# Kernel optimization log

Hardware: AMD Instinct MI355X
Metric: run time of the kernel (lower is better)

## Reference

```python
import jax, jax.numpy as jnp
import numpy as np

THRESHOLD = 0.5     # overlap_thresh
NEG_POS = 3         # negative:positive ratio
VAR = (0.1, 0.2)    # cfg['variance']


def point_form(pr):
    # cxcywh -> xmin,ymin,xmax,ymax
    return jnp.concatenate([pr[:, :2] - pr[:, 2:] / 2, pr[:, :2] + pr[:, 2:] / 2], axis=1)


def jaccard(a, b):
    # a: [N,4] point-form truths, b: [P,4] point-form priors -> IoU [N,P]
    lt = jnp.maximum(a[:, None, :2], b[None, :, :2])
    rb = jnp.minimum(a[:, None, 2:], b[None, :, 2:])
    wh = jnp.clip(rb - lt, 0.0)
    inter = wh[..., 0] * wh[..., 1]
    area_a = ((a[:, 2] - a[:, 0]) * (a[:, 3] - a[:, 1]))[:, None]
    area_b = ((b[:, 2] - b[:, 0]) * (b[:, 3] - b[:, 1]))[None, :]
    return inter / (area_a + area_b - inter)


def encode(matched, priors):
    # matched: [P,4] point-form, priors: [P,4] cxcywh
    g_cxcy = ((matched[:, :2] + matched[:, 2:]) / 2 - priors[:, :2]) / (VAR[0] * priors[:, 2:])
    g_wh = jnp.log((matched[:, 2:] - matched[:, :2]) / priors[:, 2:]) / VAR[1]
    return jnp.concatenate([g_cxcy, g_wh], axis=1)


def match_one(truths, labels, priors):
    # truths [N,4], labels [N], priors [P,4] cxcywh
    N = truths.shape[0]
    P = priors.shape[0]
    overlaps = jaccard(truths, point_form(priors))          # [N,P]
    best_prior_idx = jnp.argmax(overlaps, axis=1)           # [N] best prior per truth
    best_truth_overlap = jnp.max(overlaps, axis=0)          # [P]
    best_truth_idx = jnp.argmax(overlaps, axis=0)           # [P]
    # ensure each truth's best prior is kept (overlap forced to 2)
    best_truth_overlap = best_truth_overlap.at[best_prior_idx].set(2.0)
    hit = best_prior_idx[:, None] == jnp.arange(P)[None, :]  # [N,P]
    chosen = jnp.max(jnp.where(hit, jnp.arange(N)[:, None], -1), axis=0)
    best_truth_idx = jnp.where(chosen >= 0, chosen, best_truth_idx)
    matched = truths[best_truth_idx]                        # [P,4]
    conf = labels[best_truth_idx].astype(jnp.int32) + 1
    conf = jnp.where(best_truth_overlap < THRESHOLD, 0, conf)
    return encode(matched, priors), conf


def smooth_l1(x):
    ax = jnp.abs(x)
    return jnp.where(ax < 1.0, 0.5 * ax * ax, ax - 0.5)


def multibox_loss(loc_data, conf_data, priors, targets):
    num, P, C = conf_data.shape
    truths = targets[..., :4]
    labels = targets[..., 4]
    loc_t, conf_t = jax.vmap(match_one, in_axes=(0, 0, None))(truths, labels, priors)
    pos = conf_t > 0                                        # [B,P]

    # localization loss over positives
    loss_l = jnp.sum(jnp.where(pos[..., None], smooth_l1(loc_data - loc_t), 0.0))

    # hard-negative mining score: logsumexp - conf[label clamped to {0,1}]
    batch_conf = jax.lax.stop_gradient(conf_data).reshape(-1, C)
    conf_flat = conf_t.reshape(-1)
    clamped = jnp.where(conf_flat != 0, 1, conf_flat)
    # replicate torch nonzero()-indexing quirk: row 0 also set to 1 if any positive exists
    clamped = clamped.at[0].set(jnp.where(jnp.any(conf_flat != 0), 1, clamped[0]))
    lse = jax.scipy.special.logsumexp(batch_conf, axis=1)
    loss_c = lse - jnp.take_along_axis(batch_conf, clamped[:, None], axis=1)[:, 0]
    loss_c = loss_c.reshape(num, P)
    loss_c = jnp.where(pos, 0.0, loss_c)
    # rank of each prior by descending mining loss
    idx_rank = jnp.argsort(jnp.argsort(-loss_c, axis=1), axis=1)
    num_pos = jnp.sum(pos.astype(jnp.int32), axis=1, keepdims=True)  # [B,1]
    num_neg = jnp.clip(NEG_POS * num_pos, None, P - 1)
    neg = idx_rank < num_neg
    sel = pos | neg

    # confidence cross-entropy over selected priors, original labels as targets
    logp = jax.nn.log_softmax(conf_data, axis=-1)           # [B,P,C]
    ce = -jnp.take_along_axis(logp, conf_t[..., None], axis=-1)[..., 0]
    loss_conf = jnp.sum(jnp.where(sel, ce, 0.0))

    Nf = jnp.sum(num_pos).astype(jnp.float32)
    return loss_l / Nf, loss_conf / Nf


def setup_inputs() -> dict:
    key = jax.random.key(0)
    k1, k2, k3, k4, k5, k6, k7 = jax.random.split(key, 7)
    B, P, C, NOBJ = 128, 8732, 21, 20
    loc_data = jax.random.normal(k1, (B, P, 4), jnp.float32)
    conf_data = jax.random.normal(k2, (B, P, C), jnp.float32)
    pcxy = jax.random.uniform(k3, (P, 2), jnp.float32, 0.05, 0.95)
    pwh = jax.random.uniform(k4, (P, 2), jnp.float32, 0.05, 0.4)
    priors = jnp.concatenate([pcxy, pwh], axis=1)           # cxcywh
    mins = jax.random.uniform(k5, (B, NOBJ, 2), jnp.float32, 0.0, 0.6)
    wh = jax.random.uniform(k6, (B, NOBJ, 2), jnp.float32, 0.05, 0.35)
    lab = jax.random.randint(k7, (B, NOBJ), 0, C - 1).astype(jnp.float32)
    targets = jnp.concatenate([mins, mins + wh, lab[..., None]], axis=-1)
    return {"loc_data": loc_data, "conf_data": conf_data, "priors": priors, "targets": targets}


def reference(loc_data, conf_data, priors, targets):
    return multibox_loss(loc_data, conf_data, priors, targets)
```

## Files before the change

kernel.cpp:

```cpp
#include <hip/hip_runtime.h>

#define PP 8732
#define NB 20
#define NC 21
#define BTH 256
#define NCH 35
#define BTS 1024
#define NWS (BTS/64)

__device__ __forceinline__ float sl1(float d){
  float a = fabsf(d);
  return a < 1.0f ? 0.5f*a*a : a - 0.5f;
}

__device__ __forceinline__ float wave_max64(float x){
  int t;
  t = __builtin_amdgcn_update_dpp(0, __float_as_int(x), 0x111, 0xF, 0xF, true); x = fmaxf(x, __int_as_float(t));
  t = __builtin_amdgcn_update_dpp(0, __float_as_int(x), 0x112, 0xF, 0xF, true); x = fmaxf(x, __int_as_float(t));
  t = __builtin_amdgcn_update_dpp(0, __float_as_int(x), 0x114, 0xF, 0xF, true); x = fmaxf(x, __int_as_float(t));
  t = __builtin_amdgcn_update_dpp(0, __float_as_int(x), 0x118, 0xF, 0xF, true); x = fmaxf(x, __int_as_float(t));
  t = __builtin_amdgcn_update_dpp(0, __float_as_int(x), 0x142, 0xF, 0xF, true); x = fmaxf(x, __int_as_float(t));
  t = __builtin_amdgcn_update_dpp(0, __float_as_int(x), 0x143, 0xF, 0xF, true); x = fmaxf(x, __int_as_float(t));
  return __int_as_float(__builtin_amdgcn_readlane(__float_as_int(x), 63));
}

extern "C" __global__ void __launch_bounds__(BTH)
mb_main(const float* __restrict__ conf_data,
        const float* __restrict__ priors,
        const float* __restrict__ targets,
        float* __restrict__ rankneg,
        unsigned char* __restrict__ meta,
        unsigned long long* __restrict__ keys2)
{
  const int b = blockIdx.x, chunk = blockIdx.y;
  const int tid = threadIdx.x, lane = tid & 63, wid = tid >> 6;
  const int q0 = chunk*BTH + wid*64;
  const int cnt = (q0 < PP) ? ((PP - q0 < 64) ? (PP - q0) : 64) : 0;

  __shared__ float s_buf[4][64*NC];
  __shared__ float4 s_tr4[NB];
  __shared__ unsigned long long s_keys[4][NB];

  if (tid < NB*4){
    int n = tid>>2, k2 = tid&3;
    ((float*)s_tr4)[tid] = targets[((long)b*NB + n)*5 + k2];
  }
  if (lane < NB) s_keys[wid][lane] = 0ULL;
  __syncthreads();

  if (cnt == 64){
    const float4* cb4 = reinterpret_cast<const float4*>(conf_data + ((long)b*PP + q0)*NC);
    float4* sb4 = reinterpret_cast<float4*>(s_buf[wid]);
    #pragma unroll
    for (int ii=0; ii<6; ii++){
      int i = ii*64 + lane;
      if (i < 336) sb4[i] = cb4[i];
    }
  } else if (cnt > 0){
    const float4* cb4 = reinterpret_cast<const float4*>(conf_data + ((long)b*PP + q0)*NC);
    float4* sb4 = reinterpret_cast<float4*>(s_buf[wid]);
    const int tot4 = (cnt*NC) >> 2;
    for (int i=lane; i<tot4; i+=64) sb4[i] = cb4[i];
  }

  const bool valid = (lane < cnt);
  const int p  = q0 + lane;
  const int pl = valid ? p : 0;

  const float* v = s_buf[wid] + lane*NC;
  float m = v[0];
  #pragma unroll
  for (int c=1;c<NC;c++) m = fmaxf(m, v[c]);
  float s = 0.f;
  #pragma unroll
  for (int c=0;c<NC;c++) s += __expf(v[c]-m);
  float lse = __logf(s) + m;
  if (valid) rankneg[(long)b*PP + p] = lse - v[0];

  float4 pr = reinterpret_cast<const float4*>(priors)[pl];
  float bx1 = pr.x - pr.z*0.5f, by1 = pr.y - pr.w*0.5f;
  float bx2 = pr.x + pr.z*0.5f, by2 = pr.y + pr.w*0.5f;
  float area_b = (bx2-bx1)*(by2-by1);
  float bestov = -1.0f; int bestn = 0;

  for (int n=0;n<NB;n++){
    float4 t = s_tr4[n];
    float lx=fmaxf(t.x,bx1), ly=fmaxf(t.y,by1);
    float rx=fminf(t.z,bx2), ry=fminf(t.w,by2);
    float iw=fmaxf(rx-lx,0.f), ih=fmaxf(ry-ly,0.f);
    float inter = iw*ih;
    float aa = (t.z-t.x)*(t.w-t.y);
    float iou = inter * __builtin_amdgcn_rcpf(aa + area_b - inter);
    if (iou > bestov){ bestov=iou; bestn=n; }

    float iouv = valid ? iou : -1.0f;
    float wmax = wave_max64(iouv);
    unsigned long long mk = __ballot(valid && (iou == wmax));
    if (mk){
      int wlane = __ffsll((long long)mk) - 1;
      if (lane == wlane)
        s_keys[wid][n] = ((unsigned long long)__float_as_uint(iou)<<32)
                       | (unsigned long long)(0xFFFFFFFFu - (unsigned)p);
    }
  }

  if (valid) meta[(long)b*PP + p] = (unsigned char)((bestn<<1) | (bestov >= 0.5f ? 1 : 0));

  __syncthreads();
  if (tid < NB){
    unsigned long long mx = s_keys[0][tid];
    #pragma unroll
    for (int w=1;w<4;w++) if (s_keys[w][tid] > mx) mx = s_keys[w][tid];
    keys2[((long)b*NCH + chunk)*NB + tid] = mx;
  }
}

extern "C" __global__ void __launch_bounds__(BTS)
mb_select(const float* __restrict__ loc_data,
          const float* __restrict__ conf_data,
          const float* __restrict__ priors,
          const float* __restrict__ targets,
          const float* __restrict__ rankneg,
          const unsigned char* __restrict__ meta,
          const unsigned long long* __restrict__ keys2,
          float* __restrict__ rowres, int* __restrict__ ticket,
          float* __restrict__ out, int Bn)
{
  const int b = blockIdx.x, tid = threadIdx.x, lane = tid & 63, wid = tid >> 6;
  __shared__ float s_val[PP];
  __shared__ unsigned int s_meta4[PP/4];
  __shared__ float4 s_tr4[NB];
  __shared__ float s_lab[NB];
  __shared__ int   s_bp[NB];
  __shared__ int   s_cnt[2][NWS];
  __shared__ float s_fa[NWS], s_fb[NWS], s_fc[NWS];
  __shared__ int   s_ia[NWS];
  __shared__ float s_rowll, s_rowpc, s_delta;
  __shared__ int   s_npos, s_spec, s_last;
  unsigned char* s_meta = (unsigned char*)s_meta4;
  float4* sv4 = reinterpret_cast<float4*>(s_val);

  const float4* rr = reinterpret_cast<const float4*>(rankneg + (long)b*PP);
  for (int i=tid;i<PP/4;i+=BTS) sv4[i]=rr[i];
  const unsigned int* mr = reinterpret_cast<const unsigned int*>(meta + (long)b*PP);
  for (int i=tid;i<PP/4;i+=BTS) s_meta4[i]=mr[i];
  if (tid < NB*5){
    int n = tid/5, k2 = tid-n*5;
    float vv = targets[((long)b*NB+n)*5+k2];
    if (k2<4) ((float*)&s_tr4[n])[k2]=vv; else s_lab[n]=vv;
  }
  if (tid < NB){
    unsigned long long mx = 0ULL;
    #pragma unroll
    for (int c=0;c<NCH;c++){
      unsigned long long kk = keys2[((long)b*NCH + c)*NB + tid];
      if (kk > mx) mx = kk;
    }
    s_bp[tid] = (int)(0xFFFFFFFFu - (unsigned)(mx & 0xFFFFFFFFULL));
  }
  if (tid==0){ s_spec=0; s_delta=0.f; }
  __syncthreads();

  if (tid==0){
    for (int n=0;n<NB;n++) s_meta[s_bp[n]] = (unsigned char)((n<<1)|1);
  }
  __syncthreads();

  float ll=0.f, pc=0.f; int np=0;
  for (int p=tid;p<PP;p+=BTS){
    int mt = s_meta[p];
    if (mt & 1){
      np++;
      int n = mt>>1;
      int ct = (int)s_lab[n] + 1;
      const float* cp = conf_data + ((long)b*PP+p)*NC;
      float v0 = cp[0], vct = cp[ct];
      pc += s_val[p] + v0 - vct;
      float4 t = s_tr4[n];
      float4 pr = reinterpret_cast<const float4*>(priors)[p];
      float4 ld = reinterpret_cast<const float4*>(loc_data)[(long)b*PP+p];
      float g0 = ((t.x+t.z)*0.5f - pr.x)/(0.1f*pr.z);
      float g1 = ((t.y+t.w)*0.5f - pr.y)/(0.1f*pr.w);
      float g2 = __logf((t.z-t.x)/pr.z)/0.2f;
      float g3 = __logf((t.w-t.y)/pr.w)/0.2f;
      ll += sl1(ld.x-g0)+sl1(ld.y-g1)+sl1(ld.z-g2)+sl1(ld.w-g3);
      s_val[p] = 0.f;
    } else if (b==0 && p==0){
      float v0 = conf_data[0], v1 = conf_data[1];
      float r0 = s_val[0];
      float r0p = r0 + v0 - v1;
      s_delta = r0 - r0p;
      s_spec = 1;
      s_val[0] = r0p;
    }
  }
  #pragma unroll
  for (int o=32;o;o>>=1){
    ll += __shfl_down(ll,o,64);
    pc += __shfl_down(pc,o,64);
    np += __shfl_down(np,o,64);
  }
  if (lane==0){ s_fa[wid]=ll; s_fb[wid]=pc; s_ia[wid]=np; }
  __syncthreads();

  float4 rv0 = sv4[tid];
  float4 rv1 = sv4[tid+1024];
  float4 rv2 = (tid < PP/4-2048) ? sv4[tid+2048]
                                 : make_float4(0.f,0.f,0.f,0.f);

  if (tid==0){
    float a=0.f,c2=0.f; int ni=0;
    for (int w=0;w<NWS;w++){ a+=s_fa[w]; c2+=s_fb[w]; ni+=s_ia[w]; }
    s_rowll=a; s_rowpc=c2; s_npos=ni;
  }
  __syncthreads();
  const int num_pos = s_npos;
  int k = num_pos*3; if (k > PP-1) k = PP-1;

  float negsum = 0.f;
  if (k > 0){
    unsigned lo=0u, hi=0x7f800000u;
    int it=0;
    while (lo < hi){
      unsigned mid = lo + ((hi - lo + 1u) >> 1);
      int c = (__float_as_uint(rv0.x)>=mid) + (__float_as_uint(rv0.y)>=mid)
            + (__float_as_uint(rv0.z)>=mid) + (__float_as_uint(rv0.w)>=mid)
            + (__float_as_uint(rv1.x)>=mid) + (__float_as_uint(rv1.y)>=mid)
            + (__float_as_uint(rv1.z)>=mid) + (__float_as_uint(rv1.w)>=mid)
            + (__float_as_uint(rv2.x)>=mid) + (__float_as_uint(rv2.y)>=mid)
            + (__float_as_uint(rv2.z)>=mid) + (__float_as_uint(rv2.w)>=mid);
      #pragma unroll
      for (int o=32;o;o>>=1) c += __shfl_down(c,o,64);
      int sl2 = it&1;
      if (lane==0) s_cnt[sl2][wid]=c;
      __syncthreads();
      int tot=0;
      #pragma unroll
      for (int w=0;w<NWS;w++) tot += s_cnt[sl2][w];
      if (tot >= k) lo = mid; else hi = mid - 1u;
      it++;
    }
    const unsigned vstar = lo;

    int cg=0; float sg=0.f;
    #define ACC(x) if (__float_as_uint(x)>vstar){cg++;sg+=(x);}
    ACC(rv0.x) ACC(rv0.y) ACC(rv0.z) ACC(rv0.w)
    ACC(rv1.x) ACC(rv1.y) ACC(rv1.z) ACC(rv1.w)
    ACC(rv2.x) ACC(rv2.y) ACC(rv2.z) ACC(rv2.w)
    #undef ACC
    #pragma unroll
    for (int o=32;o;o>>=1){ cg += __shfl_down(cg,o,64); sg += __shfl_down(sg,o,64); }
    __syncthreads();
    if (lane==0){ s_ia[wid]=cg; s_fa[wid]=sg; }
    __syncthreads();
    if (tid==0){
      int cG=0; float sumG=0.f;
      for (int w=0;w<NWS;w++){ cG+=s_ia[w]; sumG+=s_fa[w]; }
      int tie = k - cG;
      negsum = sumG + (float)tie * __uint_as_float(vstar);
      if (b==0 && s_spec && __float_as_uint(s_val[0]) >= vstar) negsum += s_delta;
    }
  }

  if (tid==0){
    rowres[b*4+0] = s_rowll;
    rowres[b*4+1] = s_rowpc + negsum;
    rowres[b*4+2] = (float)num_pos;
    __threadfence();
    int t = atomicAdd(ticket, 1);
    s_last = (t == gridDim.x - 1) ? 1 : 0;
  }
  __syncthreads();

  if (s_last){
    __threadfence();
    float a0=0.f, a1=0.f, a2=0.f;
    for (int i=tid;i<Bn;i+=BTS){
      a0 += rowres[i*4+0]; a1 += rowres[i*4+1]; a2 += rowres[i*4+2];
    }
    #pragma unroll
    for (int o=32;o;o>>=1){
      a0 += __shfl_down(a0,o,64);
      a1 += __shfl_down(a1,o,64);
      a2 += __shfl_down(a2,o,64);
    }
    if (lane==0){ s_fa[wid]=a0; s_fb[wid]=a1; s_fc[wid]=a2; }
    __syncthreads();
    if (tid==0){
      float A0=0.f,A1=0.f,A2=0.f;
      for (int w=0;w<NWS;w++){ A0+=s_fa[w]; A1+=s_fb[w]; A2+=s_fc[w]; }
      out[0] = A0/A2;
      out[1] = A1/A2;
    }
  }
}

extern "C" void kernel_launch(void* const* d_in, const int* in_sizes, int n_in,
                              void* d_out, int out_size, void* d_ws, size_t ws_size,
                              hipStream_t stream) {
  const float* loc     = (const float*)d_in[0];
  const float* conf    = (const float*)d_in[1];
  const float* priors  = (const float*)d_in[2];
  const float* targets = (const float*)d_in[3];
  float* out = (float*)d_out;
  int B = in_sizes[0] / (PP*4);

  char* ws = (char*)d_ws;
  int*   ticket = (int*)ws;
  float* rowres = (float*)(ws + 64);
  unsigned long long* keys2 = (unsigned long long*)(ws + 4096);
  size_t off_rank = 4096 + (size_t)B*NCH*NB*8;
  float* rankneg = (float*)(ws + off_rank);
  unsigned char* metaa = (unsigned char*)(ws + off_rank + (size_t)B*PP*4);

  hipMemsetAsync(d_ws, 0, 64, stream);
  hipLaunchKernelGGL(mb_main,   dim3(B, NCH), dim3(BTH), 0, stream,
                     conf, priors, targets, rankneg, metaa, keys2);
  hipLaunchKernelGGL(mb_select, dim3(B), dim3(BTS), 0, stream,
                     loc, conf, priors, targets, rankneg, metaa, keys2,
                     rowres, ticket, out, B);
}
```

Baseline: 214.2 us.

## Fuse main and select kernels via per-row last-block ticket

```diff
diff --git a/kernel.cpp b/kernel.cpp
--- a/kernel.cpp
+++ b/kernel.cpp
@@ -1,12 +1,13 @@
 #include <hip/hip_runtime.h>
 
-#define PP 8732
-#define NB 20
-#define NC 21
-#define BTH 256
-#define NCH 35
-#define BTS 1024
-#define NWS (BTS/64)
+#define PP   8732
+#define PP4  2183
+#define NB   20
+#define NC   21
+#define BTH  256
+#define NCH  35
+#define NR   9
+
 
 __device__ __forceinline__ float sl1(float d){
   float a = fabsf(d);
@@ -25,12 +26,16 @@
 }
 
 extern "C" __global__ void __launch_bounds__(BTH)
-mb_main(const float* __restrict__ conf_data,
-        const float* __restrict__ priors,
-        const float* __restrict__ targets,
-        float* __restrict__ rankneg,
-        unsigned char* __restrict__ meta,
-        unsigned long long* __restrict__ keys2)
+mb_fused(const float* __restrict__ loc_data,
+         const float* __restrict__ conf_data,
+         const float* __restrict__ priors,
+         const float* __restrict__ targets,
+         int* __restrict__ gticket, int* __restrict__ rticket,
+         float* __restrict__ rowres,
+         unsigned long long* __restrict__ keys2,
+         float* __restrict__ rankneg,
+         unsigned char* __restrict__ meta,
+         float* __restrict__ out, int Bn)
 {
   const int b = blockIdx.x, chunk = blockIdx.y;
   const int tid = threadIdx.x, lane = tid & 63, wid = tid >> 6;
@@ -39,13 +44,26 @@
 
   __shared__ float s_buf[4][64*NC];
   __shared__ float4 s_tr4[NB];
+  __shared__ float  s_area[NB];
+  __shared__ float  s_lab[NB];
   __shared__ unsigned long long s_keys[4][NB];
+  __shared__ int    s_bp[NB];
+  __shared__ int    s_cnt[2][4];
+  __shared__ float  s_fa[4], s_fb[4], s_fc[4];
+  __shared__ int    s_ia[4];
+  __shared__ float  s_delta;
+  __shared__ unsigned s_v0bits;
+  __shared__ int    s_spec, s_npos, s_role, s_last;
 
   if (tid < NB*4){
     int n = tid>>2, k2 = tid&3;
     ((float*)s_tr4)[tid] = targets[((long)b*NB + n)*5 + k2];
   }
+  if (tid >= 64 && tid < 64+NB)
+    s_lab[tid-64] = targets[((long)b*NB + (tid-64))*5 + 4];
   if (lane < NB) s_keys[wid][lane] = 0ULL;
+  __syncthreads();
+  if (tid < NB) s_area[tid] = (s_tr4[tid].z - s_tr4[tid].x)*(s_tr4[tid].w - s_tr4[tid].y);
   __syncthreads();
 
   if (cnt == 64){
@@ -67,44 +85,44 @@
   const int p  = q0 + lane;
   const int pl = valid ? p : 0;
 
-  const float* v = s_buf[wid] + lane*NC;
-  float m = v[0];
-  #pragma unroll
-  for (int c=1;c<NC;c++) m = fmaxf(m, v[c]);
-  float s = 0.f;
-  #pragma unroll
-  for (int c=0;c<NC;c++) s += __expf(v[c]-m);
-  float lse = __logf(s) + m;
-  if (valid) rankneg[(long)b*PP + p] = lse - v[0];
-
-  float4 pr = reinterpret_cast<const float4*>(priors)[pl];
-  float bx1 = pr.x - pr.z*0.5f, by1 = pr.y - pr.w*0.5f;
-  float bx2 = pr.x + pr.z*0.5f, by2 = pr.y + pr.w*0.5f;
-  float area_b = (bx2-bx1)*(by2-by1);
-  float bestov = -1.0f; int bestn = 0;
-
-  for (int n=0;n<NB;n++){
-    float4 t = s_tr4[n];
-    float lx=fmaxf(t.x,bx1), ly=fmaxf(t.y,by1);
-    float rx=fminf(t.z,bx2), ry=fminf(t.w,by2);
-    float iw=fmaxf(rx-lx,0.f), ih=fmaxf(ry-ly,0.f);
-    float inter = iw*ih;
-    float aa = (t.z-t.x)*(t.w-t.y);
-    float iou = inter * __builtin_amdgcn_rcpf(aa + area_b - inter);
-    if (iou > bestov){ bestov=iou; bestn=n; }
-
-    float iouv = valid ? iou : -1.0f;
-    float wmax = wave_max64(iouv);
-    unsigned long long mk = __ballot(valid && (iou == wmax));
-    if (mk){
+  {
+    const float* v = s_buf[wid] + lane*NC;
+    float m = v[0];
+    #pragma unroll
+    for (int c=1;c<NC;c++) m = fmaxf(m, v[c]);
+    float s = 0.f;
+    #pragma unroll
+    for (int c=0;c<NC;c++) s += __expf(v[c]-m);
+    float lse = __logf(s) + m;
+    if (valid) rankneg[(long)b*PP + p] = lse - v[0];
+  }
+
+  {
+    float4 pr = reinterpret_cast<const float4*>(priors)[pl];
+    float bx1 = pr.x - pr.z*0.5f, by1 = pr.y - pr.w*0.5f;
+    float bx2 = pr.x + pr.z*0.5f, by2 = pr.y + pr.w*0.5f;
+    float area_b = (bx2-bx1)*(by2-by1);
+    float bestov = -1.0f; int bestn = 0;
+
+    for (int n=0;n<NB;n++){
+      float4 t = s_tr4[n];
+      float lx=fmaxf(t.x,bx1), ly=fmaxf(t.y,by1);
+      float rx=fminf(t.z,bx2), ry=fminf(t.w,by2);
+      float iw=fmaxf(rx-lx,0.f), ih=fmaxf(ry-ly,0.f);
+      float inter = iw*ih;
+      float iou = inter * __builtin_amdgcn_rcpf(s_area[n] + area_b - inter);
+      if (iou > bestov){ bestov=iou; bestn=n; }
+
+      float iouv = valid ? iou : -1.0f;
+      float wmax = wave_max64(iouv);
+      unsigned long long mk = __ballot(valid && (iou == wmax));
       int wlane = __ffsll((long long)mk) - 1;
       if (lane == wlane)
         s_keys[wid][n] = ((unsigned long long)__float_as_uint(iou)<<32)
                        | (unsigned long long)(0xFFFFFFFFu - (unsigned)p);
     }
-  }
-
-  if (valid) meta[(long)b*PP + p] = (unsigned char)((bestn<<1) | (bestov >= 0.5f ? 1 : 0));
+    if (valid) meta[(long)b*PP + p] = (unsigned char)((bestn<<1) | (bestov >= 0.5f ? 1 : 0));
+  }
 
   __syncthreads();
   if (tid < NB){
@@ -113,52 +131,41 @@
     for (int w=1;w<4;w++) if (s_keys[w][tid] > mx) mx = s_keys[w][tid];
     keys2[((long)b*NCH + chunk)*NB + tid] = mx;
   }
-}
-
-extern "C" __global__ void __launch_bounds__(BTS)
-mb_select(const float* __restrict__ loc_data,
-          const float* __restrict__ conf_data,
-          const float* __restrict__ priors,
-          const float* __restrict__ targets,
-          const float* __restrict__ rankneg,
-          const unsigned char* __restrict__ meta,
-          const unsigned long long* __restrict__ keys2,
-          float* __restrict__ rowres, int* __restrict__ ticket,
-          float* __restrict__ out, int Bn)
-{
-  const int b = blockIdx.x, tid = threadIdx.x, lane = tid & 63, wid = tid >> 6;
-  __shared__ float s_val[PP];
-  __shared__ unsigned int s_meta4[PP/4];
-  __shared__ float4 s_tr4[NB];
-  __shared__ float s_lab[NB];
-  __shared__ int   s_bp[NB];
-  __shared__ int   s_cnt[2][NWS];
-  __shared__ float s_fa[NWS], s_fb[NWS], s_fc[NWS];
-  __shared__ int   s_ia[NWS];
-  __shared__ float s_rowll, s_rowpc, s_delta;
-  __shared__ int   s_npos, s_spec, s_last;
-  unsigned char* s_meta = (unsigned char*)s_meta4;
-  float4* sv4 = reinterpret_cast<float4*>(s_val);
-
-  const float4* rr = reinterpret_cast<const float4*>(rankneg + (long)b*PP);
-  for (int i=tid;i<PP/4;i+=BTS) sv4[i]=rr[i];
-  const unsigned int* mr = reinterpret_cast<const unsigned int*>(meta + (long)b*PP);
-  for (int i=tid;i<PP/4;i+=BTS) s_meta4[i]=mr[i];
-  if (tid < NB*5){
-    int n = tid/5, k2 = tid-n*5;
-    float vv = targets[((long)b*NB+n)*5+k2];
-    if (k2<4) ((float*)&s_tr4[n])[k2]=vv; else s_lab[n]=vv;
-  }
+
+  __threadfence();
+  __syncthreads();
+  if (tid==0){
+    int t = atomicAdd(&rticket[b], 1);
+    s_role = (t == NCH-1) ? 1 : 0;
+  }
+  __syncthreads();
+  if (!s_role) return;
+  __threadfence();
+
   if (tid < NB){
     unsigned long long mx = 0ULL;
-    #pragma unroll
     for (int c=0;c<NCH;c++){
       unsigned long long kk = keys2[((long)b*NCH + c)*NB + tid];
       if (kk > mx) mx = kk;
     }
     s_bp[tid] = (int)(0xFFFFFFFFu - (unsigned)(mx & 0xFFFFFFFFULL));
   }
-  if (tid==0){ s_spec=0; s_delta=0.f; }
+  unsigned int* s_m4 = reinterpret_cast<unsigned int*>(&s_buf[0][0]);
+  unsigned char* s_meta = reinterpret_cast<unsigned char*>(s_m4);
+  {
+    const unsigned int* mr = reinterpret_cast<const unsigned int*>(meta + (long)b*PP);
+    for (int i=tid;i<PP4;i+=BTH) s_m4[i] = mr[i];
+  }
+  float4 rv[NR];
+  {
+    const float4* rr = reinterpret_cast<const float4*>(rankneg + (long)b*PP);
+    #pragma unroll
+    for (int j=0;j<NR;j++){
+      int i = tid + j*BTH;
+      rv[j] = (i < PP4) ? rr[i] : make_float4(0.f,0.f,0.f,0.f);
+    }
+  }
+  if (tid==0){ s_spec=0; s_delta=0.f; s_v0bits=0u; }
   __syncthreads();
 
   if (tid==0){
@@ -167,33 +174,44 @@
   __syncthreads();
 
   float ll=0.f, pc=0.f; int np=0;
-  for (int p=tid;p<PP;p+=BTS){
-    int mt = s_meta[p];
-    if (mt & 1){
-      np++;
-      int n = mt>>1;
-      int ct = (int)s_lab[n] + 1;
-      const float* cp = conf_data + ((long)b*PP+p)*NC;
-      float v0 = cp[0], vct = cp[ct];
-      pc += s_val[p] + v0 - vct;
-      float4 t = s_tr4[n];
-      float4 pr = reinterpret_cast<const float4*>(priors)[p];
-      float4 ld = reinterpret_cast<const float4*>(loc_data)[(long)b*PP+p];
-      float g0 = ((t.x+t.z)*0.5f - pr.x)/(0.1f*pr.z);
-      float g1 = ((t.y+t.w)*0.5f - pr.y)/(0.1f*pr.w);
-      float g2 = __logf((t.z-t.x)/pr.z)/0.2f;
-      float g3 = __logf((t.w-t.y)/pr.w)/0.2f;
-      ll += sl1(ld.x-g0)+sl1(ld.y-g1)+sl1(ld.z-g2)+sl1(ld.w-g3);
-      s_val[p] = 0.f;
-    } else if (b==0 && p==0){
-      float v0 = conf_data[0], v1 = conf_data[1];
-      float r0 = s_val[0];
-      float r0p = r0 + v0 - v1;
-      s_delta = r0 - r0p;
-      s_spec = 1;
-      s_val[0] = r0p;
-    }
-  }
+  #pragma unroll
+  for (int j=0;j<NR;j++){
+    int i = tid + j*BTH;
+    if (i < PP4){
+      float* rvp = (float*)&rv[j];
+      #pragma unroll
+      for (int e=0;e<4;e++){
+        int pp = 4*i + e;
+        int mt = s_meta[pp];
+        if (mt & 1){
+          np++;
+          int n = mt>>1;
+          int ct = (int)s_lab[n] + 1;
+          const float* cp = conf_data + ((long)b*PP+pp)*NC;
+          float v0 = cp[0], vct = cp[ct];
+          pc += rvp[e] + v0 - vct;
+          float4 t = s_tr4[n];
+          float4 pr = reinterpret_cast<const float4*>(priors)[pp];
+          float4 ld = reinterpret_cast<const float4*>(loc_data)[(long)b*PP+pp];
+          float g0 = ((t.x+t.z)*0.5f - pr.x)/(0.1f*pr.z);
+          float g1 = ((t.y+t.w)*0.5f - pr.y)/(0.1f*pr.w);
+          float g2 = __logf((t.z-t.x)/pr.z)/0.2f;
+          float g3 = __logf((t.w-t.y)/pr.w)/0.2f;
+          ll += sl1(ld.x-g0)+sl1(ld.y-g1)+sl1(ld.z-g2)+sl1(ld.w-g3);
+          rvp[e] = 0.f;
+        } else if (b==0 && pp==0){
+          float v0 = conf_data[0], v1 = conf_data[1];
+          float r0 = rvp[0];
+          float r0p = r0 + v0 - v1;
+          s_delta = r0 - r0p;
+          s_spec = 1;
+          rvp[0] = r0p;
+        }
+      }
+    }
+  }
+  if (tid==0) s_v0bits = __float_as_uint(rv[0].x);
+
   #pragma unroll
   for (int o=32;o;o>>=1){
     ll += __shfl_down(ll,o,64);
@@ -202,19 +220,14 @@
   }
   if (lane==0){ s_fa[wid]=ll; s_fb[wid]=pc; s_ia[wid]=np; }
   __syncthreads();
-
-  float4 rv0 = sv4[tid];
-  float4 rv1 = sv4[tid+1024];
-  float4 rv2 = (tid < PP/4-2048) ? sv4[tid+2048]
-                                 : make_float4(0.f,0.f,0.f,0.f);
-
   if (tid==0){
     float a=0.f,c2=0.f; int ni=0;
-    for (int w=0;w<NWS;w++){ a+=s_fa[w]; c2+=s_fb[w]; ni+=s_ia[w]; }
-    s_rowll=a; s_rowpc=c2; s_npos=ni;
+    for (int w=0;w<4;w++){ a+=s_fa[w]; c2+=s_fb[w]; ni+=s_ia[w]; }
+    s_fa[0]=a; s_fb[0]=c2; s_npos=ni;
   }
   __syncthreads();
   const int num_pos = s_npos;
+  const float row_ll = s_fa[0], row_pc = s_fb[0];
   int k = num_pos*3; if (k > PP-1) k = PP-1;
 
   float negsum = 0.f;
@@ -223,31 +236,31 @@
     int it=0;
     while (lo < hi){
       unsigned mid = lo + ((hi - lo + 1u) >> 1);
-      int c = (__float_as_uint(rv0.x)>=mid) + (__float_as_uint(rv0.y)>=mid)
-            + (__float_as_uint(rv0.z)>=mid) + (__float_as_uint(rv0.w)>=mid)
-            + (__float_as_uint(rv1.x)>=mid) + (__float_as_uint(rv1.y)>=mid)
-            + (__float_as_uint(rv1.z)>=mid) + (__float_as_uint(rv1.w)>=mid)
-            + (__float_as_uint(rv2.x)>=mid) + (__float_as_uint(rv2.y)>=mid)
-            + (__float_as_uint(rv2.z)>=mid) + (__float_as_uint(rv2.w)>=mid);
+      int c=0;
+      #pragma unroll
+      for (int j=0;j<NR;j++){
+        c += (__float_as_uint(rv[j].x)>=mid) + (__float_as_uint(rv[j].y)>=mid)
+           + (__float_as_uint(rv[j].z)>=mid) + (__float_as_uint(rv[j].w)>=mid);
+      }
       #pragma unroll
       for (int o=32;o;o>>=1) c += __shfl_down(c,o,64);
       int sl2 = it&1;
       if (lane==0) s_cnt[sl2][wid]=c;
       __syncthreads();
-      int tot=0;
-      #pragma unroll
-      for (int w=0;w<NWS;w++) tot += s_cnt[sl2][w];
+      int tot = s_cnt[sl2][0]+s_cnt[sl2][1]+s_cnt[sl2][2]+s_cnt[sl2][3];
       if (tot >= k) lo = mid; else hi = mid - 1u;
       it++;
     }
     const unsigned vstar = lo;
 
     int cg=0; float sg=0.f;
-    #define ACC(x) if (__float_as_uint(x)>vstar){cg++;sg+=(x);}
-    ACC(rv0.x) ACC(rv0.y) ACC(rv0.z) ACC(rv0.w)
-    ACC(rv1.x) ACC(rv1.y) ACC(rv1.z) ACC(rv1.w)
-    ACC(rv2.x) ACC(rv2.y) ACC(rv2.z) ACC(rv2.w)
-    #undef ACC
+    #pragma unroll
+    for (int j=0;j<NR;j++){
+      if (__float_as_uint(rv[j].x)>vstar){cg++;sg+=rv[j].x;}
+      if (__float_as_uint(rv[j].y)>vstar){cg++;sg+=rv[j].y;}
+      if (__float_as_uint(rv[j].z)>vstar){cg++;sg+=rv[j].z;}
+      if (__float_as_uint(rv[j].w)>vstar){cg++;sg+=rv[j].w;}
+    }
     #pragma unroll
     for (int o=32;o;o>>=1){ cg += __shfl_down(cg,o,64); sg += __shfl_down(sg,o,64); }
     __syncthreads();
@@ -255,43 +268,42 @@
     __syncthreads();
     if (tid==0){
       int cG=0; float sumG=0.f;
-      for (int w=0;w<NWS;w++){ cG+=s_ia[w]; sumG+=s_fa[w]; }
+      for (int w=0;w<4;w++){ cG+=s_ia[w]; sumG+=s_fa[w]; }
       int tie = k - cG;
       negsum = sumG + (float)tie * __uint_as_float(vstar);
-      if (b==0 && s_spec && __float_as_uint(s_val[0]) >= vstar) negsum += s_delta;
-    }
-  }
-
-  if (tid==0){
-    rowres[b*4+0] = s_rowll;
-    rowres[b*4+1] = s_rowpc + negsum;
+      if (b==0 && s_spec && s_v0bits >= vstar) negsum += s_delta;
+    }
+  }
+
+  if (tid==0){
+    rowres[b*4+0] = row_ll;
+    rowres[b*4+1] = row_pc + negsum;
     rowres[b*4+2] = (float)num_pos;
     __threadfence();
-    int t = atomicAdd(ticket, 1);
-    s_last = (t == gridDim.x - 1) ? 1 : 0;
-  }
-  __syncthreads();
-
-  if (s_last){
-    __threadfence();
-    float a0=0.f, a1=0.f, a2=0.f;
-    for (int i=tid;i<Bn;i+=BTS){
-      a0 += rowres[i*4+0]; a1 += rowres[i*4+1]; a2 += rowres[i*4+2];
-    }
-    #pragma unroll
-    for (int o=32;o;o>>=1){
-      a0 += __shfl_down(a0,o,64);
-      a1 += __shfl_down(a1,o,64);
-      a2 += __shfl_down(a2,o,64);
-    }
-    if (lane==0){ s_fa[wid]=a0; s_fb[wid]=a1; s_fc[wid]=a2; }
-    __syncthreads();
-    if (tid==0){
-      float A0=0.f,A1=0.f,A2=0.f;
-      for (int w=0;w<NWS;w++){ A0+=s_fa[w]; A1+=s_fb[w]; A2+=s_fc[w]; }
-      out[0] = A0/A2;
-      out[1] = A1/A2;
-    }
+    int t = atomicAdd(gticket, 1);
+    s_last = (t == Bn-1) ? 1 : 0;
+  }
+  __syncthreads();
+  if (!s_last) return;
+  __threadfence();
+
+  float a0=0.f, a1=0.f, a2=0.f;
+  for (int i=tid;i<Bn;i+=BTH){
+    a0 += rowres[i*4+0]; a1 += rowres[i*4+1]; a2 += rowres[i*4+2];
+  }
+  #pragma unroll
+  for (int o=32;o;o>>=1){
+    a0 += __shfl_down(a0,o,64);
+    a1 += __shfl_down(a1,o,64);
+    a2 += __shfl_down(a2,o,64);
+  }
+  if (lane==0){ s_fa[wid]=a0; s_fb[wid]=a1; s_fc[wid]=a2; }
+  __syncthreads();
+  if (tid==0){
+    float A0=0.f,A1=0.f,A2=0.f;
+    for (int w=0;w<4;w++){ A0+=s_fa[w]; A1+=s_fb[w]; A2+=s_fc[w]; }
+    out[0] = A0/A2;
+    out[1] = A1/A2;
   }
 }
 
@@ -306,17 +318,16 @@
   int B = in_sizes[0] / (PP*4);
 
   char* ws = (char*)d_ws;
-  int*   ticket = (int*)ws;
-  float* rowres = (float*)(ws + 64);
-  unsigned long long* keys2 = (unsigned long long*)(ws + 4096);
-  size_t off_rank = 4096 + (size_t)B*NCH*NB*8;
+  int*   gticket = (int*)ws;
+  int*   rticket = (int*)(ws + 64);
+  float* rowres  = (float*)(ws + 4096);
+  unsigned long long* keys2 = (unsigned long long*)(ws + 8192);
+  size_t off_rank = 8192 + (size_t)B*NCH*NB*8;
   float* rankneg = (float*)(ws + off_rank);
   unsigned char* metaa = (unsigned char*)(ws + off_rank + (size_t)B*PP*4);
 
-  hipMemsetAsync(d_ws, 0, 64, stream);
-  hipLaunchKernelGGL(mb_main,   dim3(B, NCH), dim3(BTH), 0, stream,
-                     conf, priors, targets, rankneg, metaa, keys2);
-  hipLaunchKernelGGL(mb_select, dim3(B), dim3(BTS), 0, stream,
-                     loc, conf, priors, targets, rankneg, metaa, keys2,
-                     rowres, ticket, out, B);
+  hipMemsetAsync(d_ws, 0, 4096, stream);
+  hipLaunchKernelGGL(mb_fused, dim3(B, NCH), dim3(BTH), 0, stream,
+                     loc, conf, priors, targets,
+                     gticket, rticket, rowres, keys2, rankneg, metaa, out, B);
 }
```

Result: slower. 513.8 us (+139.9%).

## Move per-truth best-prior search into dedicated blocks and drop in-loop wave reductions

Applied to the files above, without the earlier changes.

```diff
diff --git a/kernel.cpp b/kernel.cpp
--- a/kernel.cpp
+++ b/kernel.cpp
@@ -1,12 +1,14 @@
 #include <hip/hip_runtime.h>
 
-#define PP 8732
-#define NB 20
-#define NC 21
-#define BTH 256
-#define NCH 35
-#define BTS 1024
-#define NWS (BTS/64)
+#define PP   8732
+#define PP4  2183
+#define NB   20
+#define NC   21
+#define BTH  256
+#define NCH  35
+#define BTS  1024
+#define NWS  (BTS/64)
+
 
 __device__ __forceinline__ float sl1(float d){
   float a = fabsf(d);
@@ -24,29 +26,75 @@
   return __int_as_float(__builtin_amdgcn_readlane(__float_as_int(x), 63));
 }
 
+__device__ __forceinline__ int wave_min64_i32(int x){
+  int t;
+  t = __builtin_amdgcn_update_dpp(0x7FFFFFFF, x, 0x111, 0xF, 0xF, false); x = min(x, t);
+  t = __builtin_amdgcn_update_dpp(0x7FFFFFFF, x, 0x112, 0xF, 0xF, false); x = min(x, t);
+  t = __builtin_amdgcn_update_dpp(0x7FFFFFFF, x, 0x114, 0xF, 0xF, false); x = min(x, t);
+  t = __builtin_amdgcn_update_dpp(0x7FFFFFFF, x, 0x118, 0xF, 0xF, false); x = min(x, t);
+  t = __builtin_amdgcn_update_dpp(0x7FFFFFFF, x, 0x142, 0xF, 0xF, false); x = min(x, t);
+  t = __builtin_amdgcn_update_dpp(0x7FFFFFFF, x, 0x143, 0xF, 0xF, false); x = min(x, t);
+  return __builtin_amdgcn_readlane(x, 63);
+}
+
 extern "C" __global__ void __launch_bounds__(BTH)
-mb_main(const float* __restrict__ conf_data,
+mb_work(const float* __restrict__ conf_data,
         const float* __restrict__ priors,
         const float* __restrict__ targets,
         float* __restrict__ rankneg,
         unsigned char* __restrict__ meta,
-        unsigned long long* __restrict__ keys2)
+        unsigned long long* __restrict__ keys)
 {
-  const int b = blockIdx.x, chunk = blockIdx.y;
+  const int b = blockIdx.x;
   const int tid = threadIdx.x, lane = tid & 63, wid = tid >> 6;
+
+  if (blockIdx.y >= NCH){
+    const int n = blockIdx.y - NCH;
+    __shared__ unsigned long long s_k[4];
+    const float* tr = targets + ((long)b*NB + n)*5;
+    const float tx1 = tr[0], ty1 = tr[1], tx2 = tr[2], ty2 = tr[3];
+    const float aa = (tx2-tx1)*(ty2-ty1);
+    float best = -1.f; int bp = 0;
+    for (int p = tid; p < PP; p += BTH){
+      float4 pr = reinterpret_cast<const float4*>(priors)[p];
+      float bx1 = pr.x - pr.z*0.5f, by1 = pr.y - pr.w*0.5f;
+      float bx2 = pr.x + pr.z*0.5f, by2 = pr.y + pr.w*0.5f;
+      float ab = (bx2-bx1)*(by2-by1);
+      float lx=fmaxf(tx1,bx1), ly=fmaxf(ty1,by1);
+      float rx=fminf(tx2,bx2), ry=fminf(ty2,by2);
+      float iw=fmaxf(rx-lx,0.f), ih=fmaxf(ry-ly,0.f);
+      float inter = iw*ih;
+      float iou = inter * __builtin_amdgcn_rcpf(aa + ab - inter);
+      if (iou > best){ best = iou; bp = p; }
+    }
+    float wmax = wave_max64(best);
+    int cand = (best == wmax) ? bp : 0x7FFFFFFF;
+    int pmin = wave_min64_i32(cand);
+    if (lane==0)
+      s_k[wid] = ((unsigned long long)__float_as_uint(wmax)<<32)
+               | (unsigned long long)(0xFFFFFFFFu - (unsigned)pmin);
+    __syncthreads();
+    if (tid==0){
+      unsigned long long m = s_k[0];
+      #pragma unroll
+      for (int w=1;w<4;w++) if (s_k[w] > m) m = s_k[w];
+      keys[b*NB + n] = m;
+    }
+    return;
+  }
+
+  const int chunk = blockIdx.y;
   const int q0 = chunk*BTH + wid*64;
   const int cnt = (q0 < PP) ? ((PP - q0 < 64) ? (PP - q0) : 64) : 0;
 
   __shared__ float s_buf[4][64*NC];
   __shared__ float4 s_tr4[NB];
-  __shared__ unsigned long long s_keys[4][NB];
+  __shared__ float  s_area[NB];
 
   if (tid < NB*4){
     int n = tid>>2, k2 = tid&3;
     ((float*)s_tr4)[tid] = targets[((long)b*NB + n)*5 + k2];
   }
-  if (lane < NB) s_keys[wid][lane] = 0ULL;
-  __syncthreads();
 
   if (cnt == 64){
     const float4* cb4 = reinterpret_cast<const float4*>(conf_data + ((long)b*PP + q0)*NC);
@@ -62,56 +110,44 @@
     const int tot4 = (cnt*NC) >> 2;
     for (int i=lane; i<tot4; i+=64) sb4[i] = cb4[i];
   }
+  __syncthreads();
+  if (tid < NB) s_area[tid] = (s_tr4[tid].z - s_tr4[tid].x)*(s_tr4[tid].w - s_tr4[tid].y);
+  __syncthreads();
 
   const bool valid = (lane < cnt);
   const int p  = q0 + lane;
   const int pl = valid ? p : 0;
 
-  const float* v = s_buf[wid] + lane*NC;
-  float m = v[0];
-  #pragma unroll
-  for (int c=1;c<NC;c++) m = fmaxf(m, v[c]);
-  float s = 0.f;
-  #pragma unroll
-  for (int c=0;c<NC;c++) s += __expf(v[c]-m);
-  float lse = __logf(s) + m;
-  if (valid) rankneg[(long)b*PP + p] = lse - v[0];
-
-  float4 pr = reinterpret_cast<const float4*>(priors)[pl];
-  float bx1 = pr.x - pr.z*0.5f, by1 = pr.y - pr.w*0.5f;
-  float bx2 = pr.x + pr.z*0.5f, by2 = pr.y + pr.w*0.5f;
-  float area_b = (bx2-bx1)*(by2-by1);
-  float bestov = -1.0f; int bestn = 0;
-
-  for (int n=0;n<NB;n++){
-    float4 t = s_tr4[n];
-    float lx=fmaxf(t.x,bx1), ly=fmaxf(t.y,by1);
-    float rx=fminf(t.z,bx2), ry=fminf(t.w,by2);
-    float iw=fmaxf(rx-lx,0.f), ih=fmaxf(ry-ly,0.f);
-    float inter = iw*ih;
-    float aa = (t.z-t.x)*(t.w-t.y);
-    float iou = inter * __builtin_amdgcn_rcpf(aa + area_b - inter);
-    if (iou > bestov){ bestov=iou; bestn=n; }
-
-    float iouv = valid ? iou : -1.0f;
-    float wmax = wave_max64(iouv);
-    unsigned long long mk = __ballot(valid && (iou == wmax));
-    if (mk){
-      int wlane = __ffsll((long long)mk) - 1;
-      if (lane == wlane)
-        s_keys[wid][n] = ((unsigned long long)__float_as_uint(iou)<<32)
-                       | (unsigned long long)(0xFFFFFFFFu - (unsigned)p);
-    }
-  }
-
-  if (valid) meta[(long)b*PP + p] = (unsigned char)((bestn<<1) | (bestov >= 0.5f ? 1 : 0));
-
-  __syncthreads();
-  if (tid < NB){
-    unsigned long long mx = s_keys[0][tid];
+  {
+    const float* v = s_buf[wid] + lane*NC;
+    float s0=0.f, s1=0.f, s2=0.f;
     #pragma unroll
-    for (int w=1;w<4;w++) if (s_keys[w][tid] > mx) mx = s_keys[w][tid];
-    keys2[((long)b*NCH + chunk)*NB + tid] = mx;
+    for (int c=0;c<21;c+=3){
+      s0 += __expf(v[c]);
+      s1 += __expf(v[c+1]);
+      s2 += __expf(v[c+2]);
+    }
+    float lse = __logf(s0+s1+s2);
+    if (valid) rankneg[(long)b*PP + p] = lse - v[0];
+  }
+
+  {
+    float4 pr = reinterpret_cast<const float4*>(priors)[pl];
+    float bx1 = pr.x - pr.z*0.5f, by1 = pr.y - pr.w*0.5f;
+    float bx2 = pr.x + pr.z*0.5f, by2 = pr.y + pr.w*0.5f;
+    float area_b = (bx2-bx1)*(by2-by1);
+    float bestov = -1.0f; int bestn = 0;
+    #pragma unroll 4
+    for (int n=0;n<NB;n++){
+      float4 t = s_tr4[n];
+      float lx=fmaxf(t.x,bx1), ly=fmaxf(t.y,by1);
+      float rx=fminf(t.z,bx2), ry=fminf(t.w,by2);
+      float iw=fmaxf(rx-lx,0.f), ih=fmaxf(ry-ly,0.f);
+      float inter = iw*ih;
+      float iou = inter * __builtin_amdgcn_rcpf(s_area[n] + area_b - inter);
+      if (iou > bestov){ bestov=iou; bestn=n; }
+    }
+    if (valid) meta[(long)b*PP + p] = (unsigned char)((bestn<<1) | (bestov >= 0.5f ? 1 : 0));
   }
 }
 
@@ -122,41 +158,36 @@
           const float* __restrict__ targets,
           const float* __restrict__ rankneg,
           const unsigned char* __restrict__ meta,
-          const unsigned long long* __restrict__ keys2,
-          float* __restrict__ rowres, int* __restrict__ ticket,
+          const unsigned long long* __restrict__ keys,
+          float* __restrict__ rowres, int* __restrict__ gticket,
           float* __restrict__ out, int Bn)
 {
   const int b = blockIdx.x, tid = threadIdx.x, lane = tid & 63, wid = tid >> 6;
   __shared__ float s_val[PP];
-  __shared__ unsigned int s_meta4[PP/4];
+  __shared__ unsigned int s_meta4[PP4];
   __shared__ float4 s_tr4[NB];
   __shared__ float s_lab[NB];
   __shared__ int   s_bp[NB];
   __shared__ int   s_cnt[2][NWS];
   __shared__ float s_fa[NWS], s_fb[NWS], s_fc[NWS];
   __shared__ int   s_ia[NWS];
-  __shared__ float s_rowll, s_rowpc, s_delta;
+  __shared__ float s_delta;
   __shared__ int   s_npos, s_spec, s_last;
   unsigned char* s_meta = (unsigned char*)s_meta4;
   float4* sv4 = reinterpret_cast<float4*>(s_val);
 
   const float4* rr = reinterpret_cast<const float4*>(rankneg + (long)b*PP);
-  for (int i=tid;i<PP/4;i+=BTS) sv4[i]=rr[i];
+  for (int i=tid;i<PP4;i+=BTS) sv4[i]=rr[i];
   const unsigned int* mr = reinterpret_cast<const unsigned int*>(meta + (long)b*PP);
-  for (int i=tid;i<PP/4;i+=BTS) s_meta4[i]=mr[i];
+  for (int i=tid;i<PP4;i+=BTS) s_meta4[i]=mr[i];
   if (tid < NB*5){
     int n = tid/5, k2 = tid-n*5;
     float vv = targets[((long)b*NB+n)*5+k2];
     if (k2<4) ((float*)&s_tr4[n])[k2]=vv; else s_lab[n]=vv;
   }
   if (tid < NB){
-    unsigned long long mx = 0ULL;
-    #pragma unroll
-    for (int c=0;c<NCH;c++){
-      unsigned long long kk = keys2[((long)b*NCH + c)*NB + tid];
-      if (kk > mx) mx = kk;
-    }
-    s_bp[tid] = (int)(0xFFFFFFFFu - (unsigned)(mx & 0xFFFFFFFFULL));
+    unsigned long long kk = keys[b*NB + tid];
+    s_bp[tid] = (int)(0xFFFFFFFFu - (unsigned)(kk & 0xFFFFFFFFULL));
   }
   if (tid==0){ s_spec=0; s_delta=0.f; }
   __syncthreads();
@@ -205,16 +236,17 @@
 
   float4 rv0 = sv4[tid];
   float4 rv1 = sv4[tid+1024];
-  float4 rv2 = (tid < PP/4-2048) ? sv4[tid+2048]
+  float4 rv2 = (tid < PP4-2048) ? sv4[tid+2048]
                                  : make_float4(0.f,0.f,0.f,0.f);
 
   if (tid==0){
     float a=0.f,c2=0.f; int ni=0;
     for (int w=0;w<NWS;w++){ a+=s_fa[w]; c2+=s_fb[w]; ni+=s_ia[w]; }
-    s_rowll=a; s_rowpc=c2; s_npos=ni;
+    s_fa[0]=a; s_fb[0]=c2; s_npos=ni;
   }
   __syncthreads();
   const int num_pos = s_npos;
+  const float row_ll = s_fa[0], row_pc = s_fb[0];
   int k = num_pos*3; if (k > PP-1) k = PP-1;
 
   float negsum = 0.f;
@@ -263,35 +295,34 @@
   }
 
   if (tid==0){
-    rowres[b*4+0] = s_rowll;
-    rowres[b*4+1] = s_rowpc + negsum;
+    rowres[b*4+0] = row_ll;
+    rowres[b*4+1] = row_pc + negsum;
     rowres[b*4+2] = (float)num_pos;
     __threadfence();
-    int t = atomicAdd(ticket, 1);
-    s_last = (t == gridDim.x - 1) ? 1 : 0;
-  }
-  __syncthreads();
-
-  if (s_last){
-    __threadfence();
-    float a0=0.f, a1=0.f, a2=0.f;
-    for (int i=tid;i<Bn;i+=BTS){
-      a0 += rowres[i*4+0]; a1 += rowres[i*4+1]; a2 += rowres[i*4+2];
-    }
-    #pragma unroll
-    for (int o=32;o;o>>=1){
-      a0 += __shfl_down(a0,o,64);
-      a1 += __shfl_down(a1,o,64);
-      a2 += __shfl_down(a2,o,64);
-    }
-    if (lane==0){ s_fa[wid]=a0; s_fb[wid]=a1; s_fc[wid]=a2; }
-    __syncthreads();
-    if (tid==0){
-      float A0=0.f,A1=0.f,A2=0.f;
-      for (int w=0;w<NWS;w++){ A0+=s_fa[w]; A1+=s_fb[w]; A2+=s_fc[w]; }
-      out[0] = A0/A2;
-      out[1] = A1/A2;
-    }
+    int t = atomicAdd(gticket, 1);
+    s_last = (t == Bn-1) ? 1 : 0;
+  }
+  __syncthreads();
+  if (!s_last) return;
+  __threadfence();
+
+  float a0=0.f, a1=0.f, a2=0.f;
+  for (int i=tid;i<Bn;i+=BTS){
+    a0 += rowres[i*4+0]; a1 += rowres[i*4+1]; a2 += rowres[i*4+2];
+  }
+  #pragma unroll
+  for (int o=32;o;o>>=1){
+    a0 += __shfl_down(a0,o,64);
+    a1 += __shfl_down(a1,o,64);
+    a2 += __shfl_down(a2,o,64);
+  }
+  if (lane==0){ s_fa[wid]=a0; s_fb[wid]=a1; s_fc[wid]=a2; }
+  __syncthreads();
+  if (tid==0){
+    float A0=0.f,A1=0.f,A2=0.f;
+    for (int w=0;w<NWS;w++){ A0+=s_fa[w]; A1+=s_fb[w]; A2+=s_fc[w]; }
+    out[0] = A0/A2;
+    out[1] = A1/A2;
   }
 }
 
@@ -306,17 +337,16 @@
   int B = in_sizes[0] / (PP*4);
 
   char* ws = (char*)d_ws;
-  int*   ticket = (int*)ws;
-  float* rowres = (float*)(ws + 64);
-  unsigned long long* keys2 = (unsigned long long*)(ws + 4096);
-  size_t off_rank = 4096 + (size_t)B*NCH*NB*8;
-  float* rankneg = (float*)(ws + off_rank);
-  unsigned char* metaa = (unsigned char*)(ws + off_rank + (size_t)B*PP*4);
+  int*   gticket = (int*)ws;
+  float* rowres  = (float*)(ws + 256);
+  unsigned long long* keys = (unsigned long long*)(ws + 4096);
+  float* rankneg = (float*)(ws + 32768);
+  unsigned char* metaa = (unsigned char*)(ws + 32768 + (size_t)B*PP*4);
 
   hipMemsetAsync(d_ws, 0, 64, stream);
-  hipLaunchKernelGGL(mb_main,   dim3(B, NCH), dim3(BTH), 0, stream,
-                     conf, priors, targets, rankneg, metaa, keys2);
+  hipLaunchKernelGGL(mb_work, dim3(B, NCH+NB), dim3(BTH), 0, stream,
+                     conf, priors, targets, rankneg, metaa, keys);
   hipLaunchKernelGGL(mb_select, dim3(B), dim3(BTS), 0, stream,
-                     loc, conf, priors, targets, rankneg, metaa, keys2,
-                     rowres, ticket, out, B);
-}
+                     loc, conf, priors, targets, rankneg, metaa, keys,
+                     rowres, gticket, out, B);
+}
```

Result: no change. 216.9 us (+1.3%).
